# Kernel tuning notes

Measured on AMD Instinct MI355X. Metric: run time of the kernel, lower is better.

The kernel has to match this reference:

```python
import jax, jax.numpy as jnp
import numpy as np

# Model constants (from init_kwargs)
N_ATOMS = 30000
N_PAIRS = 300000
NF_IN = 64
NF_OUT = 64
N_DIST = 20
MIND_SOFT = 0.85
MAXD_SOFT = 5.0
HARD_CUTOFF = 6.5


def setup_inputs() -> dict:
    key = jax.random.key(0)
    k = jax.random.split(key, 8)
    in_features = jax.random.normal(k[0], (N_ATOMS, NF_IN), dtype=jnp.float32)
    pair_first = jax.random.randint(k[1], (N_PAIRS,), 0, N_ATOMS)
    pair_second = jax.random.randint(k[2], (N_PAIRS,), 0, N_ATOMS)
    dist_pairs = jax.random.uniform(k[3], (N_PAIRS,), dtype=jnp.float32,
                                    minval=MIND_SOFT, maxval=HARD_CUTOFF)
    # InverseSensitivityModule init: mu uniformly spaced in inverse-distance space
    mu = jnp.linspace(1.0 / MAXD_SOFT, 1.0 / MIND_SOFT, N_DIST, dtype=jnp.float32)
    sigma = jnp.full((N_DIST,), (1.0 / MIND_SOFT - 1.0 / MAXD_SOFT) / N_DIST,
                     dtype=jnp.float32)
    # xavier-normal-ish init scales
    int_weights = jax.random.normal(k[4], (N_DIST, NF_OUT, NF_IN), dtype=jnp.float32) \
        * np.sqrt(2.0 / (NF_IN + NF_OUT)).astype(np.float32)
    w_self = jax.random.normal(k[5], (NF_OUT, NF_IN), dtype=jnp.float32) \
        * np.sqrt(2.0 / (NF_IN + NF_OUT)).astype(np.float32)
    b_self = jax.random.normal(k[6], (NF_OUT,), dtype=jnp.float32) * 0.01
    return {"in_features": in_features, "pair_first": pair_first,
            "pair_second": pair_second, "dist_pairs": dist_pairs,
            "mu": mu, "sigma": sigma, "int_weights": int_weights,
            "w_self": w_self, "b_self": b_self}


def _sensitivity(dist, mu, sigma):
    # Inverse-distance Gaussian sensitivities with smooth cosine hard cutoff.
    inv_d = 1.0 / dist  # [P]
    gauss = jnp.exp(-0.5 * ((inv_d[:, None] - mu[None, :]) / sigma[None, :]) ** 2)  # [P, n_dist]
    cut = jnp.cos(0.5 * jnp.pi * dist / HARD_CUTOFF) ** 2
    cut = jnp.where(dist < HARD_CUTOFF, cut, 0.0)
    return gauss * cut[:, None]


def reference(in_features, pair_first, pair_second, dist_pairs,
              mu, sigma, int_weights, w_self, b_self):
    n_atoms = in_features.shape[0]
    sense = _sensitivity(dist_pairs, mu, sigma)              # [P, n_dist]
    # envsum: env[a, nu, f] = sum_{p: pair_first[p]==a} sense[p, nu] * in_features[pair_second[p], f]
    neigh = in_features[pair_second]                          # [P, nf_in] gather
    contrib = sense[:, :, None] * neigh[:, None, :]           # [P, n_dist, nf_in]
    env = jax.ops.segment_sum(
        contrib.reshape(contrib.shape[0], N_DIST * NF_IN),
        pair_first, num_segments=n_atoms)                     # [A, n_dist*nf_in]
    # interaction matmul: weights permuted (n_dist, nf_in, nf_out) then flattened
    weights_rs = jnp.transpose(int_weights, (0, 2, 1)).reshape(N_DIST * NF_IN, NF_OUT)
    features_out = env @ weights_rs                           # [A, nf_out]
    features_out += in_features @ w_self.T + b_self           # self interaction
    return features_out
```

## Files before the change

### kernel.cpp

```cpp
#include <hip/hip_runtime.h>
#include <math.h>

#define N_ATOMS    30000
#define N_PAIRS    300000
#define CAP        48
#define NF         64
#define ND         20
#define K_ENV      1280
#define K_TOT      1344
#define NKSTEP     42
#define HARD_CUT   6.5f
#define BA         16
#define ESTRIDE    1352
#define D_LO       0.85f
#define D_SCALE    (5.65f / 65535.0f)
#define D_SCALE_I  (65535.0f / 5.65f)
#define NM1        ((unsigned)(N_ATOMS - 1))

typedef short    s16x8  __attribute__((ext_vector_type(8)));
typedef __bf16   bf16x8 __attribute__((ext_vector_type(8)));
typedef unsigned u32x4  __attribute__((ext_vector_type(4)));
typedef float    f32x4  __attribute__((ext_vector_type(4)));
typedef float    f32x16 __attribute__((ext_vector_type(16)));

__device__ __forceinline__ unsigned short f2bf(float x) {
    union { float f; unsigned u; } v; v.f = x;
    unsigned r = v.u + 0x7fffu + ((v.u >> 16) & 1u);
    return (unsigned short)(r >> 16);
}
__device__ __forceinline__ unsigned pkbf(float a, float b) {
    return (unsigned)f2bf(a) | ((unsigned)f2bf(b) << 16);
}
__device__ __forceinline__ float senseval(unsigned pu, int kidx, int cnt,
                                          float isig, float musig, bool nuok) {
    float d  = D_LO + (float)(pu & 0xffffu) * D_SCALE;
    float z  = __builtin_amdgcn_rcpf(d) * isig - musig;
    float co = __cosf(0.2416609733530613f * d);
    float e  = __expf(-0.5f * z * z) * (co * co);
    return (nuok && kidx < cnt) ? e : 0.0f;
}

__global__ void k_prep(const float* __restrict__ iw, const float* __restrict__ wself,
                       const float* __restrict__ mu, const float* __restrict__ sigma,
                       const float* __restrict__ x,
                       unsigned short* __restrict__ WtB, int* __restrict__ cnts,
                       float2* __restrict__ msr, unsigned* __restrict__ xb16) {
    if (blockIdx.x < 42) {
        int idx = blockIdx.x * 256 + threadIdx.x;
        if (idx >= NKSTEP * 4 * 64) return;
        int l  = idx & 63;
        int q  = (idx >> 6) & 3;
        int ks = idx >> 8;
        int n  = q * 16 + (l & 15);
        int kb = ks * 32 + (l >> 4) * 8;
        u32x4 u;
        #pragma unroll
        for (int jj = 0; jj < 4; jj++) {
            unsigned short lo, hi;
            #pragma unroll
            for (int e = 0; e < 2; e++) {
                int k = kb + 2 * jj + e;
                float val;
                if (k < K_ENV) {
                    int t  = k / 640;
                    int rm = k - t * 640;
                    int g  = rm >> 7;
                    int c  = (rm & 127) >> 2;
                    int r  = k & 3;
                    int nu = 4 * g + r;
                    int f  = 2 * c + t;
                    val = iw[(nu * NF + n) * NF + f];
                } else {
                    val = wself[n * NF + (k - K_ENV)];
                }
                if (e == 0) lo = f2bf(val); else hi = f2bf(val);
            }
            u[jj] = (unsigned)lo | ((unsigned)hi << 16);
        }
        *(u32x4*)&WtB[idx * 8] = u;
    } else if (blockIdx.x < 160) {
        int i = (blockIdx.x - 42) * 256 + threadIdx.x;
        if (i < N_ATOMS) cnts[i] = 0;
    } else if (blockIdx.x == 160) {
        int i = threadIdx.x;
        if (i < ND) { float2 m; m.x = mu[i]; m.y = 1.0f / sigma[i]; msr[i] = m; }
    } else {
        int o = (blockIdx.x - 161) * 256 + threadIdx.x;
        if (o < N_ATOMS * 32 / 4) {
            int wbase = o * 4;
            const float* src = &x[(size_t)wbase * 2];
            float2 f0 = *(const float2*)(src);
            float2 f1 = *(const float2*)(src + 2);
            float2 f2 = *(const float2*)(src + 4);
            float2 f3 = *(const float2*)(src + 6);
            u32x4 u;
            u[0] = pkbf(f0.x, f0.y);
            u[1] = pkbf(f1.x, f1.y);
            u[2] = pkbf(f2.x, f2.y);
            u[3] = pkbf(f3.x, f3.y);
            *(u32x4*)&xb16[wbase] = u;
        }
    }
}

__global__ void k_scatter(const int* __restrict__ first, const int* __restrict__ second,
                          const float* __restrict__ dist, int* __restrict__ cnts,
                          unsigned* __restrict__ pk) {
    int p = (blockIdx.x * 256 + threadIdx.x) * 2;
    if (p >= N_PAIRS) return;
    int2   f2 = *(const int2*)&first[p];
    int2   s2 = *(const int2*)&second[p];
    float2 d2 = *(const float2*)&dist[p];
    {
        int pos = atomicAdd(&cnts[f2.x], 1);
        if (pos < CAP) {
            unsigned du = min((unsigned)((d2.x - D_LO) * D_SCALE_I + 0.5f), 65535u);
            pk[(size_t)f2.x * CAP + pos] = ((unsigned)s2.x << 16) | du;
        }
    }
    {
        int pos = atomicAdd(&cnts[f2.y], 1);
        if (pos < CAP) {
            unsigned du = min((unsigned)((d2.y - D_LO) * D_SCALE_I + 0.5f), 65535u);
            pk[(size_t)f2.y * CAP + pos] = ((unsigned)s2.y << 16) | du;
        }
    }
}

__global__ void __launch_bounds__(512, 6)
k_main(const unsigned* __restrict__ xb16, const int* __restrict__ cnts,
       const unsigned* __restrict__ pk, const float2* __restrict__ msr,
       const unsigned short* __restrict__ WtB, const float* __restrict__ bself,
       float* __restrict__ out) {
    __shared__ unsigned short env[BA * ESTRIDE];
    const int t  = threadIdx.x;
    const int w  = t >> 6;
    const int l  = t & 63;
    const int h  = l >> 5;
    const int cl = l & 31;
    const int a0 = blockIdx.x * BA;

    float2 ms   = msr[min(cl, ND - 1)];
    const float isig  = ms.y;
    const float musig = ms.x * ms.y;
    const bool  nuok  = (cl < ND);
    const unsigned* xw = xb16 + cl;

    #pragma unroll 1
    for (int ci = 0; ci < 2; ci++) {
        const int i = 2 * w + ci;
        const int a = a0 + i;
        const int cnt = min(cnts[a], CAP);
        const int nst = max((cnt + 15) >> 4, 1);
        const unsigned* gb = &pk[(size_t)a * CAP];
        f32x16 acc0 = {0.f}, acc1 = {0.f};
        #pragma unroll 1
        for (int ks = 0; ks < nst; ks++) {
            const int k0 = ks * 16 + h * 8;
            uint4 p0 = *(const uint4*)(gb + k0);
            uint4 p1 = *(const uint4*)(gb + k0 + 4);
            unsigned g0 = xw[min(p0.x >> 16, NM1) * 32];
            unsigned g1 = xw[min(p0.y >> 16, NM1) * 32];
            unsigned g2 = xw[min(p0.z >> 16, NM1) * 32];
            unsigned g3 = xw[min(p0.w >> 16, NM1) * 32];
            unsigned g4 = xw[min(p1.x >> 16, NM1) * 32];
            unsigned g5 = xw[min(p1.y >> 16, NM1) * 32];
            unsigned g6 = xw[min(p1.z >> 16, NM1) * 32];
            unsigned g7 = xw[min(p1.w >> 16, NM1) * 32];
            u32x4 A, B0, B1;
            A[0] = pkbf(senseval(p0.x, k0 + 0, cnt, isig, musig, nuok),
                        senseval(p0.y, k0 + 1, cnt, isig, musig, nuok));
            A[1] = pkbf(senseval(p0.z, k0 + 2, cnt, isig, musig, nuok),
                        senseval(p0.w, k0 + 3, cnt, isig, musig, nuok));
            A[2] = pkbf(senseval(p1.x, k0 + 4, cnt, isig, musig, nuok),
                        senseval(p1.y, k0 + 5, cnt, isig, musig, nuok));
            A[3] = pkbf(senseval(p1.z, k0 + 6, cnt, isig, musig, nuok),
                        senseval(p1.w, k0 + 7, cnt, isig, musig, nuok));
            B0[0] = __builtin_amdgcn_perm(g1, g0, 0x05040100u);
            B0[1] = __builtin_amdgcn_perm(g3, g2, 0x05040100u);
            B0[2] = __builtin_amdgcn_perm(g5, g4, 0x05040100u);
            B0[3] = __builtin_amdgcn_perm(g7, g6, 0x05040100u);
            B1[0] = __builtin_amdgcn_perm(g1, g0, 0x07060302u);
            B1[1] = __builtin_amdgcn_perm(g3, g2, 0x07060302u);
            B1[2] = __builtin_amdgcn_perm(g5, g4, 0x07060302u);
            B1[3] = __builtin_amdgcn_perm(g7, g6, 0x07060302u);
            acc0 = __builtin_amdgcn_mfma_f32_32x32x16_bf16(
                       __builtin_bit_cast(bf16x8, A),
                       __builtin_bit_cast(bf16x8, B0), acc0, 0, 0, 0);
            acc1 = __builtin_amdgcn_mfma_f32_32x32x16_bf16(
                       __builtin_bit_cast(bf16x8, A),
                       __builtin_bit_cast(bf16x8, B1), acc1, 0, 0, 0);
        }
        unsigned short* er = &env[i * ESTRIDE];
        #pragma unroll
        for (int q = 0; q < 3; q++) {
            int g = 2 * q + h;
            if (g < 5) {
                uint2 v0, v1;
                v0.x = pkbf(acc0[4 * q + 0], acc0[4 * q + 1]);
                v0.y = pkbf(acc0[4 * q + 2], acc0[4 * q + 3]);
                v1.x = pkbf(acc1[4 * q + 0], acc1[4 * q + 1]);
                v1.y = pkbf(acc1[4 * q + 2], acc1[4 * q + 3]);
                *(uint2*)&er[g * 128 + cl * 4]       = v0;
                *(uint2*)&er[640 + g * 128 + cl * 4] = v1;
            }
        }
        unsigned sw = xb16[(size_t)a * 32 + (l >> 1)];
        er[K_ENV + l] = (unsigned short)(sw >> ((l & 1) * 16));
    }
    __syncthreads();

    if (w < 4) {
        const int m16  = l & 15;
        const int quad = l >> 4;
        f32x4 acc = {0.f, 0.f, 0.f, 0.f};
        for (int ks = 0; ks < NKSTEP; ks++) {
            s16x8 afrag = *(const s16x8*)&env[m16 * ESTRIDE + ks * 32 + quad * 8];
            s16x8 bfrag = *(const s16x8*)&WtB[((ks * 4 + w) * 64 + l) * 8];
            acc = __builtin_amdgcn_mfma_f32_16x16x32_bf16(
                      __builtin_bit_cast(bf16x8, afrag),
                      __builtin_bit_cast(bf16x8, bfrag), acc, 0, 0, 0);
        }
        const float bs = bself[w * 16 + m16];
        #pragma unroll
        for (int r = 0; r < 4; r++) {
            int row = quad * 4 + r;
            out[(size_t)(a0 + row) * NF + w * 16 + m16] = acc[r] + bs;
        }
    }
}

extern "C" void kernel_launch(void* const* d_in, const int* in_sizes, int n_in,
                              void* d_out, int out_size, void* d_ws, size_t ws_size,
                              hipStream_t stream) {
    const float* x      = (const float*)d_in[0];
    const int*   first  = (const int*)d_in[1];
    const int*   second = (const int*)d_in[2];
    const float* dist   = (const float*)d_in[3];
    const float* mu     = (const float*)d_in[4];
    const float* sigma  = (const float*)d_in[5];
    const float* iw     = (const float*)d_in[6];
    const float* wself  = (const float*)d_in[7];
    const float* bself  = (const float*)d_in[8];
    float* out = (float*)d_out;

    char* ws = (char*)d_ws;
    unsigned short* WtB  = (unsigned short*)(ws);
    int*            cnts = (int*)(ws + 172032);
    float2*         msr  = (float2*)(ws + 292032);
    unsigned*       pk   = (unsigned*)(ws + 292192);
    unsigned*       xb16 = (unsigned*)(ws + 6052192);

    k_prep<<<dim3(161 + (N_ATOMS * 8 + 255) / 256), dim3(256), 0, stream>>>(
        iw, wself, mu, sigma, x, WtB, cnts, msr, xb16);
    k_scatter<<<dim3((N_PAIRS / 2 + 255) / 256), dim3(256), 0, stream>>>(
        first, second, dist, cnts, pk);
    k_main<<<dim3(N_ATOMS / BA), dim3(512), 0, stream>>>(
        xb16, cnts, pk, msr, WtB, bself, out);
}
```

Before: 125.4 us.

## Precompute inverse distance and log-cutoff per pair in scatter, simplify sense eval

The scatter kernel now quantizes the inverse distance instead of the distance and stores log2 of the squared cosine cutoff alongside each packed pair, doubling the per-pair record to 8 bytes. The main kernel's sensitivity evaluation drops the reciprocal, cosine and separate multiply, leaving an FMA-based Gaussian exponent plus a single exp2. Each pair's work is done once in scatter rather than redundantly across the 20 distance-basis lanes. In exchange the main loop reads twice as many bytes of pair data, and the neighbor counts are hoisted out of the atom loop.

```diff
diff --git a/kernel.cpp b/kernel.cpp
--- a/kernel.cpp
+++ b/kernel.cpp
@@ -12,10 +12,13 @@
 #define HARD_CUT   6.5f
 #define BA         16
 #define ESTRIDE    1352
-#define D_LO       0.85f
-#define D_SCALE    (5.65f / 65535.0f)
-#define D_SCALE_I  (65535.0f / 5.65f)
 #define NM1        ((unsigned)(N_ATOMS - 1))
+
+#define INVD_LO    0.15384615385f
+#define INVD_RANGE 1.02262443439f
+#define QS         (65535.0f / INVD_RANGE)
+#define DQ         (INVD_RANGE / 65535.0f)
+#define NEXP2      (-0.7213475204444817f)
 
 typedef short    s16x8  __attribute__((ext_vector_type(8)));
 typedef __bf16   bf16x8 __attribute__((ext_vector_type(8)));
@@ -31,12 +34,12 @@
 __device__ __forceinline__ unsigned pkbf(float a, float b) {
     return (unsigned)f2bf(a) | ((unsigned)f2bf(b) << 16);
 }
-__device__ __forceinline__ float senseval(unsigned pu, int kidx, int cnt,
-                                          float isig, float musig, bool nuok) {
-    float d  = D_LO + (float)(pu & 0xffffu) * D_SCALE;
-    float z  = __builtin_amdgcn_rcpf(d) * isig - musig;
-    float co = __cosf(0.2416609733530613f * d);
-    float e  = __expf(-0.5f * z * z) * (co * co);
+__device__ __forceinline__ float senseval(unsigned w0, unsigned lcb, int kidx, int cnt,
+                                          float zA, float zB, bool nuok) {
+    float uu = (float)(w0 & 0xffffu);
+    float z  = __builtin_fmaf(uu, zA, zB);
+    float ar = __builtin_fmaf(z * z, NEXP2, __uint_as_float(lcb));
+    float e  = __builtin_amdgcn_exp2f(ar);
     return (nuok && kidx < cnt) ? e : 0.0f;
 }
 
@@ -105,31 +108,43 @@
 
 __global__ void k_scatter(const int* __restrict__ first, const int* __restrict__ second,
                           const float* __restrict__ dist, int* __restrict__ cnts,
-                          unsigned* __restrict__ pk) {
+                          uint2* __restrict__ pk) {
     int p = (blockIdx.x * 256 + threadIdx.x) * 2;
     if (p >= N_PAIRS) return;
     int2   f2 = *(const int2*)&first[p];
     int2   s2 = *(const int2*)&second[p];
     float2 d2 = *(const float2*)&dist[p];
     {
+        float d    = d2.x;
+        float invd = 1.0f / d;
+        float tq   = fmaxf((invd - INVD_LO) * QS + 0.5f, 0.0f);
+        unsigned u = min((unsigned)tq, 65535u);
+        float co   = __cosf(0.2416609733530613f * d);
+        float lc   = fmaxf(__log2f(co * co), -10000.0f);
         int pos = atomicAdd(&cnts[f2.x], 1);
         if (pos < CAP) {
-            unsigned du = min((unsigned)((d2.x - D_LO) * D_SCALE_I + 0.5f), 65535u);
-            pk[(size_t)f2.x * CAP + pos] = ((unsigned)s2.x << 16) | du;
+            uint2 v; v.x = ((unsigned)s2.x << 16) | u; v.y = __float_as_uint(lc);
+            pk[(size_t)f2.x * CAP + pos] = v;
         }
     }
     {
+        float d    = d2.y;
+        float invd = 1.0f / d;
+        float tq   = fmaxf((invd - INVD_LO) * QS + 0.5f, 0.0f);
+        unsigned u = min((unsigned)tq, 65535u);
+        float co   = __cosf(0.2416609733530613f * d);
+        float lc   = fmaxf(__log2f(co * co), -10000.0f);
         int pos = atomicAdd(&cnts[f2.y], 1);
         if (pos < CAP) {
-            unsigned du = min((unsigned)((d2.y - D_LO) * D_SCALE_I + 0.5f), 65535u);
-            pk[(size_t)f2.y * CAP + pos] = ((unsigned)s2.y << 16) | du;
+            uint2 v; v.x = ((unsigned)s2.y << 16) | u; v.y = __float_as_uint(lc);
+            pk[(size_t)f2.y * CAP + pos] = v;
         }
     }
 }
 
 __global__ void __launch_bounds__(512, 6)
 k_main(const unsigned* __restrict__ xb16, const int* __restrict__ cnts,
-       const unsigned* __restrict__ pk, const float2* __restrict__ msr,
+       const uint2* __restrict__ pk, const float2* __restrict__ msr,
        const unsigned short* __restrict__ WtB, const float* __restrict__ bself,
        float* __restrict__ out) {
     __shared__ unsigned short env[BA * ESTRIDE];
@@ -141,41 +156,48 @@
     const int a0 = blockIdx.x * BA;
 
     float2 ms   = msr[min(cl, ND - 1)];
-    const float isig  = ms.y;
-    const float musig = ms.x * ms.y;
-    const bool  nuok  = (cl < ND);
+    const float isig = ms.y;
+    const float zA   = DQ * isig;
+    const float zB   = INVD_LO * isig - ms.x * isig;
+    const bool  nuok = (cl < ND);
     const unsigned* xw = xb16 + cl;
+
+    const int cntA = min(cnts[a0 + 2 * w + 0], CAP);
+    const int cntB = min(cnts[a0 + 2 * w + 1], CAP);
 
     #pragma unroll 1
     for (int ci = 0; ci < 2; ci++) {
         const int i = 2 * w + ci;
         const int a = a0 + i;
-        const int cnt = min(cnts[a], CAP);
+        const int cnt = ci ? cntB : cntA;
         const int nst = max((cnt + 15) >> 4, 1);
-        const unsigned* gb = &pk[(size_t)a * CAP];
+        const uint2* gb = &pk[(size_t)a * CAP];
         f32x16 acc0 = {0.f}, acc1 = {0.f};
         #pragma unroll 1
         for (int ks = 0; ks < nst; ks++) {
             const int k0 = ks * 16 + h * 8;
-            uint4 p0 = *(const uint4*)(gb + k0);
-            uint4 p1 = *(const uint4*)(gb + k0 + 4);
-            unsigned g0 = xw[min(p0.x >> 16, NM1) * 32];
-            unsigned g1 = xw[min(p0.y >> 16, NM1) * 32];
-            unsigned g2 = xw[min(p0.z >> 16, NM1) * 32];
-            unsigned g3 = xw[min(p0.w >> 16, NM1) * 32];
-            unsigned g4 = xw[min(p1.x >> 16, NM1) * 32];
-            unsigned g5 = xw[min(p1.y >> 16, NM1) * 32];
-            unsigned g6 = xw[min(p1.z >> 16, NM1) * 32];
-            unsigned g7 = xw[min(p1.w >> 16, NM1) * 32];
+            const uint2* bp = gb + k0;
+            uint4 q0 = *(const uint4*)(bp + 0);
+            uint4 q1 = *(const uint4*)(bp + 2);
+            uint4 q2 = *(const uint4*)(bp + 4);
+            uint4 q3 = *(const uint4*)(bp + 6);
+            unsigned g0 = xw[min(q0.x >> 16, NM1) * 32];
+            unsigned g1 = xw[min(q0.z >> 16, NM1) * 32];
+            unsigned g2 = xw[min(q1.x >> 16, NM1) * 32];
+            unsigned g3 = xw[min(q1.z >> 16, NM1) * 32];
+            unsigned g4 = xw[min(q2.x >> 16, NM1) * 32];
+            unsigned g5 = xw[min(q2.z >> 16, NM1) * 32];
+            unsigned g6 = xw[min(q3.x >> 16, NM1) * 32];
+            unsigned g7 = xw[min(q3.z >> 16, NM1) * 32];
             u32x4 A, B0, B1;
-            A[0] = pkbf(senseval(p0.x, k0 + 0, cnt, isig, musig, nuok),
-                        senseval(p0.y, k0 + 1, cnt, isig, musig, nuok));
-            A[1] = pkbf(senseval(p0.z, k0 + 2, cnt, isig, musig, nuok),
-                        senseval(p0.w, k0 + 3, cnt, isig, musig, nuok));
-            A[2] = pkbf(senseval(p1.x, k0 + 4, cnt, isig, musig, nuok),
-                        senseval(p1.y, k0 + 5, cnt, isig, musig, nuok));
-            A[3] = pkbf(senseval(p1.z, k0 + 6, cnt, isig, musig, nuok),
-                        senseval(p1.w, k0 + 7, cnt, isig, musig, nuok));
+            A[0] = pkbf(senseval(q0.x, q0.y, k0 + 0, cnt, zA, zB, nuok),
+                        senseval(q0.z, q0.w, k0 + 1, cnt, zA, zB, nuok));
+            A[1] = pkbf(senseval(q1.x, q1.y, k0 + 2, cnt, zA, zB, nuok),
+                        senseval(q1.z, q1.w, k0 + 3, cnt, zA, zB, nuok));
+            A[2] = pkbf(senseval(q2.x, q2.y, k0 + 4, cnt, zA, zB, nuok),
+                        senseval(q2.z, q2.w, k0 + 5, cnt, zA, zB, nuok));
+            A[3] = pkbf(senseval(q3.x, q3.y, k0 + 6, cnt, zA, zB, nuok),
+                        senseval(q3.z, q3.w, k0 + 7, cnt, zA, zB, nuok));
             B0[0] = __builtin_amdgcn_perm(g1, g0, 0x05040100u);
             B0[1] = __builtin_amdgcn_perm(g3, g2, 0x05040100u);
             B0[2] = __builtin_amdgcn_perm(g5, g4, 0x05040100u);
@@ -248,8 +270,8 @@
     unsigned short* WtB  = (unsigned short*)(ws);
     int*            cnts = (int*)(ws + 172032);
     float2*         msr  = (float2*)(ws + 292032);
-    unsigned*       pk   = (unsigned*)(ws + 292192);
-    unsigned*       xb16 = (unsigned*)(ws + 6052192);
+    uint2*          pk   = (uint2*)(ws + 292192);
+    unsigned*       xb16 = (unsigned*)(ws + 11812192);
 
     k_prep<<<dim3(161 + (N_ATOMS * 8 + 255) / 256), dim3(256), 0, stream>>>(
         iw, wself, mu, sigma, x, WtB, cnts, msr, xb16);
```

New measurement: 125.8 us. No clear change (+0.3%).
